# Kernel optimization log

Measured on AMD Instinct MI355X. Metric: run time of the kernel, lower is better.

Reference implementation:

```python
import jax, jax.numpy as jnp
import numpy as np
from jax import lax

DIM = 192
HEADS = 8
B, H, W = 8, 128, 128


def dwconv3x3(x, w):
    # x: [B,C,H,W], w: [C,1,3,3] depthwise (groups=C)
    return lax.conv_general_dilated(
        x, w, window_strides=(1, 1), padding='SAME',
        feature_group_count=x.shape[1],
        dimension_numbers=('NCHW', 'OIHW', 'NCHW'))


def conv1x1(x, w, b=None):
    # w: [Cout, Cin]
    y = jnp.einsum('oc,bchw->bohw', w, x)
    if b is not None:
        y = y + b[None, :, None, None]
    return y


def setup_inputs() -> dict:
    key = jax.random.key(0)
    ks = jax.random.split(key, 9)
    s = 0.02
    return {
        'x': jax.random.normal(ks[0], (B, DIM, H, W), jnp.float32),
        'w_qkv': jax.random.normal(ks[1], (3 * DIM, DIM), jnp.float32) * s,
        'b_qkv': jnp.zeros((3 * DIM,), jnp.float32),
        'w_dw': jax.random.normal(ks[2], (3 * DIM, 1, 3, 3), jnp.float32) * s,
        'b_dw': jnp.zeros((3 * DIM,), jnp.float32),
        'w_proj': jax.random.normal(ks[3], (DIM, DIM), jnp.float32) * s,
        'b_proj': jnp.zeros((DIM,), jnp.float32),
        'w_pos1': jax.random.normal(ks[4], (DIM, 1, 3, 3), jnp.float32) * s,
        'w_pos2': jax.random.normal(ks[5], (DIM, 1, 3, 3), jnp.float32) * s,
        'temperature': jnp.ones((HEADS, 1, 1), jnp.float32),
    }


def reference(x, w_qkv, b_qkv, w_dw, b_dw, w_proj, b_proj, w_pos1, w_pos2, temperature):
    b, c, h, w = x.shape
    heads = HEADS
    ch = c // heads

    qkv = conv1x1(x, w_qkv, b_qkv)
    qkv = dwconv3x3(qkv, w_dw) + b_dw[None, :, None, None]
    q_inp, k_inp, v_inp = jnp.split(qkv, 3, axis=1)

    def to_heads(t):  # [B,C,H,W] -> [B,heads,ch,HW]
        return t.reshape(b, heads, ch, h * w)

    q = to_heads(q_inp)
    k = to_heads(k_inp)
    v = to_heads(v_inp)

    # L2 normalize over hw (torch F.normalize, eps=1e-12)
    q = q / jnp.maximum(jnp.linalg.norm(q, axis=-1, keepdims=True), 1e-12)
    k = k / jnp.maximum(jnp.linalg.norm(k, axis=-1, keepdims=True), 1e-12)

    attn = jnp.einsum('bhce,bhde->bhcd', q, k) * temperature  # [B,heads,ch,ch]
    attn = jax.nn.softmax(attn, axis=-1)
    out = jnp.einsum('bhcd,bhde->bhce', attn, v)  # [B,heads,ch,HW]
    out = out.reshape(b, c, h, w)

    out = conv1x1(out, w_proj, b_proj)

    pos = dwconv3x3(v_inp, w_pos1)
    pos = jax.nn.gelu(pos, approximate=False)
    pos = dwconv3x3(pos, w_pos2)

    return out + pos
```

## Files before the change

### kernel.cpp

```cpp
#include <hip/hip_runtime.h>
#include <stdint.h>
#include <stddef.h>

#define NB 8
#define CC 192
#define C3 576
#define HGT 128
#define WID 128
#define HW 16384
#define NH 8
#define QKROW 49152

typedef short bf16x8 __attribute__((ext_vector_type(8)));
typedef float f32x4 __attribute__((ext_vector_type(4)));

__device__ __forceinline__ unsigned short f2bf(float f) {
  unsigned int u = __float_as_uint(f);
  u += 0x7fffu + ((u >> 16) & 1u);
  return (unsigned short)(u >> 16);
}
__device__ __forceinline__ float bf2f(unsigned short h) {
  return __uint_as_float(((unsigned int)h) << 16);
}
__device__ __forceinline__ float bflo(unsigned int v) {
  return __uint_as_float(v << 16);
}
__device__ __forceinline__ float bfhi(unsigned int v) {
  return __uint_as_float(v & 0xffff0000u);
}
__device__ __forceinline__ unsigned int pk2(float a, float b) {
  return (unsigned int)f2bf(a) | ((unsigned int)f2bf(b) << 16);
}
__device__ __forceinline__ void gl_lds16(const void* g, void* l) {
  __builtin_amdgcn_global_load_lds(
      (const __attribute__((address_space(1))) unsigned int*)(uintptr_t)g,
      (__attribute__((address_space(3))) unsigned int*)(uint32_t)(uintptr_t)l,
      16, 0, 0);
}
__device__ __forceinline__ int xcd_swz(int g, int n) {
  return (g & 7) * (n >> 3) + (g >> 3);
}

__global__ __launch_bounds__(256) void ktrans(const float* __restrict__ x,
                                              unsigned char* __restrict__ xT) {
  __shared__ __align__(16) float lx[192 * 68];
  int wg = xcd_swz(blockIdx.x, gridDim.x);
  int pt = wg & 255, b = wg >> 8;
  int p0 = pt * 64;
  int tid = threadIdx.x;
#pragma unroll
  for (int i = 0; i < 12; ++i) {
    int f = tid + i * 256;
    int ic = f >> 4, q = f & 15;
    float4 v = *(const float4*)(x + ((size_t)(b * CC + ic)) * HW + p0 + q * 4);
    *(float4*)(lx + ic * 68 + q * 4) = v;
  }
  __syncthreads();
#pragma unroll
  for (int i = 0; i < 6; ++i) {
    int f = i * 256 + tid;
    int s = f >> 6, p = f & 63;
    unsigned int wv[4];
#pragma unroll
    for (int j = 0; j < 4; ++j)
      wv[j] = pk2(lx[(s * 8 + 2 * j) * 68 + p], lx[(s * 8 + 2 * j + 1) * 68 + p]);
    uint4 st; st.x = wv[0]; st.y = wv[1]; st.z = wv[2]; st.w = wv[3];
    *(uint4*)(xT + (((size_t)(b * 24 + s)) * HW + p0 + p) * 16) = st;
  }
}

__global__ void kwprep(const float* __restrict__ wq, unsigned char* __restrict__ wb) {
  int f = blockIdx.x * 256 + threadIdx.x;
  if (f >= C3 * 24) return;
  int oc = f / 24, s = f % 24;
  unsigned int wv[4];
#pragma unroll
  for (int j = 0; j < 4; ++j)
    wv[j] = pk2(wq[oc * 192 + s * 8 + 2 * j], wq[oc * 192 + s * 8 + 2 * j + 1]);
  uint4 st; st.x = wv[0]; st.y = wv[1]; st.z = wv[2]; st.w = wv[3];
  *(uint4*)(wb + (size_t)oc * 384 + ((s ^ (oc & 7)) * 16)) = st;
}

__global__ __launch_bounds__(256) void kconv1(const unsigned char* __restrict__ xT,
                                              const unsigned char* __restrict__ wb,
                                              const float* __restrict__ bqkv,
                                              unsigned short* __restrict__ vout,
                                              unsigned char* __restrict__ qkout) {
  __shared__ __align__(16) unsigned char lds[81920];
  const int TRO = 73728;
  int wg = xcd_swz(blockIdx.x, gridDim.x);
  int ot = wg % 9; int rest = wg / 9; int grp = rest & 63; int b = rest >> 6;
  int tid = threadIdx.x;
  const unsigned char* gB = wb + (size_t)ot * 24576;
#pragma unroll
  for (int i = 0; i < 6; ++i)
    gl_lds16(gB + i * 4096 + tid * 16, lds + 49152 + i * 4096 + tid * 16);
  const unsigned char* gA = xT + (size_t)b * 24 * HW * 16;
  int t0 = grp * 4;
  {
    int p0 = t0 * 64;
#pragma unroll
    for (int i = 0; i < 6; ++i) {
      int f = i * 256 + tid;
      gl_lds16(gA + (((size_t)(f >> 6)) * HW + p0 + (f & 63)) * 16, lds + f * 16);
    }
  }
  int lane = tid & 63, w = tid >> 6;
  int l15 = lane & 15, gq = lane >> 4;
  int pw = w * 16;
  int part = ot / 3, cm0 = (ot % 3) * 64;
  bool isq = (ot < 6);
  float bias[4];
#pragma unroll
  for (int nf = 0; nf < 4; ++nf) bias[nf] = bqkv[ot * 64 + nf * 16 + l15];
  size_t vbase[4];
  if (!isq) {
#pragma unroll
    for (int nf = 0; nf < 4; ++nf)
      vbase[nf] = ((size_t)(b * CC + cm0 + nf * 16 + l15)) * HW * 2;
  }
  unsigned char* qkbase = qkout + ((size_t)((part * 8 + b) * 128)) * QKROW;
  int unitw = w * 2 + (gq >> 1);
  int sub8 = (gq & 1) * 8;

  for (int it = 0; it < 4; ++it) {
    int tile = t0 + it;
    asm volatile("s_waitcnt vmcnt(0)" ::: "memory");
    __syncthreads();
    int nb = it & 1;
    if (it < 3) {
      int p1 = (tile + 1) * 64;
#pragma unroll
      for (int i = 0; i < 6; ++i) {
        int f = i * 256 + tid;
        gl_lds16(gA + (((size_t)(f >> 6)) * HW + p1 + (f & 63)) * 16,
                 lds + ((nb ^ 1) * 24576) + f * 16);
      }
    }
    f32x4 acc[4];
#pragma unroll
    for (int nf = 0; nf < 4; ++nf) acc[nf] = (f32x4){0.f, 0.f, 0.f, 0.f};
#pragma unroll
    for (int kk = 0; kk < 6; ++kk) {
      bf16x8 a = *(const bf16x8*)(lds + nb * 24576 + ((((kk * 4 + gq) << 6) + pw + l15) * 16));
      int cb = kk * 64 + gq * 16;
#pragma unroll
      for (int nf = 0; nf < 4; ++nf) {
        int r = nf * 16 + l15;
        bf16x8 bfr = *(const bf16x8*)(lds + 49152 + r * 384 + (cb ^ ((r & 7) << 4)));
        acc[nf] = __builtin_amdgcn_mfma_f32_16x16x32_bf16(a, bfr, acc[nf], 0, 0, 0);
      }
    }
    if (isq) {
#pragma unroll
      for (int nf = 0; nf < 4; ++nf) {
        int c = nf * 16 + l15;
        uint2 st;
        st.x = pk2(acc[nf][0] + bias[nf], acc[nf][1] + bias[nf]);
        st.y = pk2(acc[nf][2] + bias[nf], acc[nf][3] + bias[nf]);
        *(uint2*)(lds + TRO + c * 128 + ((unitw ^ (c & 7)) * 16) + sub8) = st;
      }
      asm volatile("s_waitcnt lgkmcnt(0)" ::: "memory");
      __builtin_amdgcn_s_barrier();
      {
        int y = tile >> 1, xh = (tile & 1) * 8;
        int u = tid >> 5, c0 = tid & 31, c1 = c0 + 32;
        uint4 v0 = *(const uint4*)(lds + TRO + c0 * 128 + ((u ^ (c0 & 7)) * 16));
        uint4 v1 = *(const uint4*)(lds + TRO + c1 * 128 + ((u ^ (c1 & 7)) * 16));
        unsigned char* grow = qkbase + (size_t)y * QKROW + (xh + u) * 3072 + cm0 * 16;
        *(uint4*)(grow + c0 * 16) = v0;
        *(uint4*)(grow + c1 * 16) = v1;
      }
    } else {
      int p = tile * 64 + pw + gq * 4;
#pragma unroll
      for (int nf = 0; nf < 4; ++nf) {
        uint2 st;
        st.x = pk2(acc[nf][0] + bias[nf], acc[nf][1] + bias[nf]);
        st.y = pk2(acc[nf][2] + bias[nf], acc[nf][3] + bias[nf]);
        *(uint2*)((unsigned char*)vout + vbase[nf] + (size_t)p * 2) = st;
      }
    }
  }
}

__global__ __launch_bounds__(256) void kqk(const unsigned char* __restrict__ qk,
                                           const float* __restrict__ wdw,
                                           const float* __restrict__ bdw,
                                           float* __restrict__ G,
                                           float* __restrict__ nq,
                                           float* __restrict__ nk) {
  __shared__ __align__(16) unsigned char lds[81920];
  const int FB = 49152;
  int wg = xcd_swz(blockIdx.x, gridDim.x);
  int band = wg & 63, h = (wg >> 6) & 7, b = wg >> 9;
  int y0 = band * 2;
  int tid = threadIdx.x;
#pragma unroll
  for (int i = 0; i < 12; ++i) {
    int f = i * 256 + tid;
    int p = f / 1536, rem = f % 1536;
    int r = rem / 384, unit = rem % 384;
    int uc = unit / 24, ch = unit % 24;
    int y = y0 - 1 + r;
    if (y >= 0 && y < HGT)
      gl_lds16(qk + ((size_t)((p * 8 + b) * 128 + y)) * QKROW + uc * 3072 + (h * 24 + ch) * 16,
               lds + f * 16);
    else
      *(uint4*)(lds + f * 16) = (uint4){0, 0, 0, 0};
  }
  asm volatile("s_waitcnt vmcnt(0)" ::: "memory");
  __syncthreads();

  int lane = tid & 63, w = tid >> 6;
  if (tid < 192) {
    int p = tid / 96; int r3m = tid % 96;
    int ch = r3m >> 2; int row = (r3m >> 1) & 1; int half = r3m & 1;
    int gc = p * 192 + h * 24 + ch;
    float wv[9];
#pragma unroll
    for (int j = 0; j < 9; ++j) wv[j] = wdw[gc * 9 + j];
    float bias = bdw[gc];
    const unsigned char* sbase = lds + p * 24576 + ch * 16;
    unsigned char* fb = lds + FB + p * 16384 + ch * 16;
    int h8 = half * 8;
    unsigned int W[3][16];
#define LOADU(dy_, m_, u_) { \
    uint4 tt = ((u_) >= 0 && (u_) < 16) \
        ? *(const uint4*)(sbase + (row + (dy_)) * 6144 + (u_) * 384) \
        : (uint4){0, 0, 0, 0}; \
    W[dy_][(m_) * 4 + 0] = tt.x; W[dy_][(m_) * 4 + 1] = tt.y; \
    W[dy_][(m_) * 4 + 2] = tt.z; W[dy_][(m_) * 4 + 3] = tt.w; }
#pragma unroll
    for (int dy = 0; dy < 3; ++dy) {
#pragma unroll
      for (int m = 0; m < 4; ++m) { LOADU(dy, m, h8 - 1 + m); }
    }
    float nsum = 0.f;
#pragma unroll
    for (int c4 = 0; c4 < 4; ++c4) {
      if (c4 > 0) {
#pragma unroll
        for (int dy = 0; dy < 3; ++dy) {
#pragma unroll
          for (int e = 0; e < 8; ++e) W[dy][e] = W[dy][8 + e];
          LOADU(dy, 2, h8 - 1 + c4 * 2 + 2);
          LOADU(dy, 3, h8 - 1 + c4 * 2 + 3);
        }
      }
      float acc[16];
#pragma unroll
      for (int j = 0; j < 16; ++j) acc[j] = bias;
#pragma unroll
      for (int dy = 0; dy < 3; ++dy) {
        float f[18];
#pragma unroll
        for (int t2 = 0; t2 < 18; ++t2) {
          int rel = 7 + t2;
          unsigned int v = W[dy][rel >> 1];
          f[t2] = (rel & 1) ? bfhi(v) : bflo(v);
        }
#pragma unroll
        for (int j = 0; j < 16; ++j)
          acc[j] += f[j] * wv[dy * 3] + f[j + 1] * wv[dy * 3 + 1] + f[j + 2] * wv[dy * 3 + 2];
      }
#pragma unroll
      for (int j = 0; j < 16; ++j) nsum += acc[j] * acc[j];
      unsigned int pk[8];
#pragma unroll
      for (int e = 0; e < 8; ++e) pk[e] = pk2(acc[2 * e], acc[2 * e + 1]);
      int kt = row * 4 + half * 2 + (c4 >> 1);
      int gb = (c4 & 1) * 2;
      uint4 s0; s0.x = pk[0]; s0.y = pk[1]; s0.z = pk[2]; s0.w = pk[3];
      uint4 s1; s1.x = pk[4]; s1.y = pk[5]; s1.z = pk[6]; s1.w = pk[7];
      *(uint4*)(fb + kt * 2048 + gb * 512) = s0;
      *(uint4*)(fb + kt * 2048 + (gb + 1) * 512) = s1;
    }
#undef LOADU
    nsum += __shfl_xor(nsum, 1);
    nsum += __shfl_xor(nsum, 2);
    if ((tid & 3) == 0) {
      float* dst = (p == 0) ? nq : nk;
      atomicAdd(dst + (b * NH + h) * 24 + ch, nsum);
    }
  } else {
    int t2 = tid - 192;
#pragma unroll
    for (int i = 0; i < 8; ++i) {
      int f = i * 64 + t2;
      int ch8 = f & 7, gq4 = (f >> 3) & 3, kt8 = (f >> 5) & 7, pp = f >> 8;
      *(uint4*)(lds + FB + pp * 16384 + kt8 * 2048 + gq4 * 512 + (24 + ch8) * 16) =
          (uint4){0, 0, 0, 0};
    }
  }
  __syncthreads();

  int l15 = lane & 15, gq = lane >> 4;
  f32x4 acc2[2][2];
#pragma unroll
  for (int ct = 0; ct < 2; ++ct)
#pragma unroll
    for (int dt = 0; dt < 2; ++dt) acc2[ct][dt] = (f32x4){0.f, 0.f, 0.f, 0.f};
#pragma unroll
  for (int t2 = 0; t2 < 2; ++t2) {
    int kt = w * 2 + t2;
    bf16x8 aq[2], bk[2];
#pragma unroll
    for (int ct = 0; ct < 2; ++ct) {
      aq[ct] = *(const bf16x8*)(lds + FB + kt * 2048 + gq * 512 + (ct * 16 + l15) * 16);
      bk[ct] = *(const bf16x8*)(lds + FB + 16384 + kt * 2048 + gq * 512 + (ct * 16 + l15) * 16);
    }
#pragma unroll
    for (int ct = 0; ct < 2; ++ct)
#pragma unroll
      for (int dt = 0; dt < 2; ++dt)
        acc2[ct][dt] = __builtin_amdgcn_mfma_f32_16x16x32_bf16(aq[ct], bk[dt], acc2[ct][dt], 0, 0, 0);
  }
  float* gp = (float*)lds;
#pragma unroll
  for (int ct = 0; ct < 2; ++ct)
#pragma unroll
    for (int dt = 0; dt < 2; ++dt)
      *(f32x4*)(gp + (((w * 4 + ct * 2 + dt) * 64) + lane) * 4) = acc2[ct][dt];
  __syncthreads();
  float* Gb = G + (size_t)(b * NH + h) * 576;
#pragma unroll
  for (int ii = 0; ii < 3; ++ii) {
    int f = ii * 256 + tid;
    if (f < 576) {
      int c = f / 24, d = f % 24;
      int t4 = ((c >> 4) << 1) + (d >> 4);
      int lane16 = (d & 15) + (((c & 15) >> 2) << 4);
      int reg = c & 3;
      float s = 0.f;
#pragma unroll
      for (int w4 = 0; w4 < 4; ++w4)
        s += gp[((w4 * 4 + t4) * 64 + lane16) * 4 + reg];
      atomicAdd(Gb + f, s);
    }
  }
}

__global__ __launch_bounds__(256) void kdwv(const unsigned short* __restrict__ src,
                                            const float* __restrict__ wdw,
                                            const float* __restrict__ bdw,
                                            unsigned char* __restrict__ vT) {
  __shared__ __align__(16) unsigned int smem[8 * 721];
  int wg = xcd_swz(blockIdx.x, gridDim.x);
  int cg = wg % 24, rt = (wg / 24) & 15, b = wg / 384;
  int y0 = rt * 8, chg0 = cg * 8;
  int tid = threadIdx.x;
  for (int i = tid; i < 5768; i += 256) smem[i] = 0;
  __syncthreads();
#pragma unroll
  for (int i = 0; i < 5; ++i) {
    int f = i * 256 + tid;
    int ch = f / 160, rem = f % 160;
    int r = rem >> 4, seg = rem & 15;
    int y = y0 - 1 + r;
    if (y >= 0 && y < HGT) {
      uint4 v = *(const uint4*)(src + ((size_t)(b * CC + chg0 + ch)) * HW + y * WID + seg * 8);
      unsigned int* dp = smem + ch * 721 + r * 72 + 4 + seg * 4;
      dp[0] = v.x; dp[1] = v.y; dp[2] = v.z; dp[3] = v.w;
    }
  }
  __syncthreads();
  int ch = tid >> 5, u = tid & 31;
  int row = u >> 2, xs = (u & 3) * 32;
  int gch = 384 + chg0 + ch;
  float wv[9];
#pragma unroll
  for (int j = 0; j < 9; ++j) wv[j] = wdw[gch * 9 + j];
  float bias = bdw[gch];
  float outv[32];
  const unsigned int* tb = smem + ch * 721;
#pragma unroll
  for (int g = 0; g < 4; ++g) {
    int x0 = xs + g * 8;
    float v[3][12];
#pragma unroll
    for (int dy = 0; dy < 3; ++dy) {
      const unsigned int* rp = tb + (row + dy) * 72 + ((x0 + 6) >> 1);
#pragma unroll
      for (int m = 0; m < 6; ++m) {
        unsigned int w2 = rp[m];
        v[dy][2 * m] = bf2f((unsigned short)(w2 & 0xffff));
        v[dy][2 * m + 1] = bf2f((unsigned short)(w2 >> 16));
      }
    }
#pragma unroll
    for (int j = 0; j < 8; ++j) {
      float a = bias;
#pragma unroll
      for (int dy = 0; dy < 3; ++dy)
#pragma unroll
        for (int dx = 0; dx < 3; ++dx)
          a += v[dy][j + dx + 1] * wv[dy * 3 + dx];
      outv[g * 8 + j] = a;
    }
  }
  __syncthreads();
  unsigned short* vt = (unsigned short*)smem;
#pragma unroll
  for (int g = 0; g < 4; ++g)
#pragma unroll
    for (int j = 0; j < 8; j += 2) {
      int x = xs + g * 8 + j;
      ((unsigned int*)smem)[ch * 512 + row * 64 + (x >> 1)] =
          pk2(outv[g * 8 + j], outv[g * 8 + j + 1]);
    }
  __syncthreads();
#pragma unroll
  for (int i = 0; i < 4; ++i) {
    int f = i * 256 + tid;
    int r = f >> 7, col = f & 127;
    unsigned int wvp[4];
#pragma unroll
    for (int e = 0; e < 4; ++e) {
      unsigned short a = vt[(2 * e) * 1024 + r * 128 + col];
      unsigned short bb = vt[(2 * e + 1) * 1024 + r * 128 + col];
      wvp[e] = (unsigned int)a | ((unsigned int)bb << 16);
    }
    uint4 st; st.x = wvp[0]; st.y = wvp[1]; st.z = wvp[2]; st.w = wvp[3];
    *(uint4*)(vT + (((size_t)(b * 24 + cg)) * HW + (size_t)(y0 + r) * WID + col) * 16) = st;
  }
}

__global__ __launch_bounds__(256) void kattn(const float* __restrict__ G,
                                             const float* __restrict__ nq,
                                             const float* __restrict__ nk,
                                             const float* __restrict__ temp,
                                             const float* __restrict__ wproj,
                                             unsigned char* __restrict__ W2) {
  __shared__ float attn[24][24];
  __shared__ float iq[24], ik[24];
  int bh = blockIdx.x;
  int h = bh & 7, b = bh >> 3;
  int tid = threadIdx.x;
  const float* Gb = G + (size_t)bh * 576;
  if (tid < 24) { float n = sqrtf(nq[bh * 24 + tid]); iq[tid] = 1.f / fmaxf(n, 1e-12f); }
  else if (tid < 48) { float n = sqrtf(nk[bh * 24 + tid - 24]); ik[tid - 24] = 1.f / fmaxf(n, 1e-12f); }
  __syncthreads();
  if (tid < 24) {
    float tmp = temp[h];
    float row[24];
    float mx = -1e30f;
#pragma unroll
    for (int d = 0; d < 24; ++d) {
      row[d] = Gb[tid * 24 + d] * iq[tid] * ik[d] * tmp;
      mx = fmaxf(mx, row[d]);
    }
    float sum = 0.f;
#pragma unroll
    for (int d = 0; d < 24; ++d) { float e = expf(row[d] - mx); row[d] = e; sum += e; }
    float inv = 1.f / sum;
#pragma unroll
    for (int d = 0; d < 24; ++d) attn[tid][d] = row[d] * inv;
  }
  __syncthreads();
  for (int i = 0; i < 18; ++i) {
    int f = tid + i * 256;
    if (f >= 4608) break;
    int oc = f / 24, d = f % 24;
    float s = 0.f;
#pragma unroll
    for (int c = 0; c < 24; ++c) s += wproj[oc * 192 + h * 24 + c] * attn[c][d];
    int gg = h * 24 + d;
    *(unsigned short*)(W2 + ((size_t)b * CC + oc) * 384 + ((gg * 2) ^ ((oc & 7) << 4))) = f2bf(s);
  }
}

__global__ __launch_bounds__(256) void kpos(const unsigned char* __restrict__ vT,
                                            const float* __restrict__ w1,
                                            const float* __restrict__ w2,
                                            unsigned short* __restrict__ pos) {
  __shared__ unsigned int vbuf[8 * 865];
  __shared__ unsigned int d1[8 * 721];
  int wg = xcd_swz(blockIdx.x, gridDim.x);
  int cg = wg % 24, rt = (wg / 24) & 15, b = wg / 384;
  int y0 = rt * 8, g0 = cg * 8;
  int tid = threadIdx.x;
  for (int i = tid; i < 6920; i += 256) vbuf[i] = 0;
  __syncthreads();
#pragma unroll
  for (int i = 0; i < 3; ++i) {
    int f = i * 256 + tid;
    int r = f >> 6, colp = f & 63;
    int y = y0 - 2 + r;
    if (y >= 0 && y < HGT) {
      const unsigned char* base = vT + (((size_t)(b * 24 + cg)) * HW + (size_t)y * WID + colp * 2) * 16;
      uint4 va = *(const uint4*)(base);
      uint4 vb2 = *(const uint4*)(base + 16);
      unsigned int la[4] = {va.x, va.y, va.z, va.w};
      unsigned int lb[4] = {vb2.x, vb2.y, vb2.z, vb2.w};
#pragma unroll
      for (int e = 0; e < 8; ++e) {
        unsigned int a16 = (la[e >> 1] >> ((e & 1) * 16)) & 0xffff;
        unsigned int b16 = (lb[e >> 1] >> ((e & 1) * 16)) & 0xffff;
        vbuf[e * 865 + r * 72 + colp + 4] = a16 | (b16 << 16);
      }
    }
  }
  __syncthreads();
  int ch = tid >> 5, u = tid & 31;
  {
    const float* wp = w1 + (g0 + ch) * 9;
    float wl[9];
#pragma unroll
    for (int j = 0; j < 9; ++j) wl[j] = wp[j];
    int x0 = u * 4;
    for (int rr = 0; rr < 10; ++rr) {
      int y = y0 - 1 + rr;
      unsigned int o0 = 0, o1 = 0;
      if (y >= 0 && y < HGT) {
        float v[3][8];
#pragma unroll
        for (int dy = 0; dy < 3; ++dy) {
          const unsigned int* rp = vbuf + ch * 865 + (rr + dy) * 72 + ((x0 + 6) >> 1);
#pragma unroll
          for (int m = 0; m < 4; ++m) {
            unsigned int w2r = rp[m];
            v[dy][2 * m] = bf2f((unsigned short)(w2r & 0xffff));
            v[dy][2 * m + 1] = bf2f((unsigned short)(w2r >> 16));
          }
        }
        float g4[4];
#pragma unroll
        for (int j = 0; j < 4; ++j) {
          float a = 0.f;
#pragma unroll
          for (int dy = 0; dy < 3; ++dy)
#pragma unroll
            for (int dx = 0; dx < 3; ++dx)
              a += v[dy][j + dx + 1] * wl[dy * 3 + dx];
          g4[j] = 0.5f * a * (1.f + erff(a * 0.70710678118f));
        }
        o0 = pk2(g4[0], g4[1]);
        o1 = pk2(g4[2], g4[3]);
      }
      unsigned int* dp = d1 + ch * 721 + rr * 72 + ((x0 + 8) >> 1);
      dp[0] = o0; dp[1] = o1;
    }
  }
  if (tid < 160) {
    int ech = tid / 20, rem = tid % 20;
    int rr = rem >> 1, side = rem & 1;
    int x = side ? 128 : -1;
    int y = y0 - 1 + rr;
    unsigned short val = 0;
    if (y >= 0 && y < HGT) {
      const float* wp = w1 + (g0 + ech) * 9;
      float a = 0.f;
      const unsigned short* vb16 = (const unsigned short*)(vbuf + ech * 865);
#pragma unroll
      for (int dy = 0; dy < 3; ++dy)
#pragma unroll
        for (int dx = 0; dx < 3; ++dx)
          a += bf2f(vb16[(rr + dy) * 144 + (x + dx + 7)]) * wp[dy * 3 + dx];
      val = f2bf(0.5f * a * (1.f + erff(a * 0.70710678118f)));
    }
    ((unsigned short*)(d1 + ech * 721))[rr * 144 + (x + 8)] = val;
  }
  __syncthreads();
  {
    const float* wp = w2 + (g0 + ch) * 9;
    float wl[9];
#pragma unroll
    for (int j = 0; j < 9; ++j) wl[j] = wp[j];
    int row = u >> 2, xs = (u & 3) * 32;
    size_t rb = ((size_t)(b * CC + g0 + ch)) * HW + (size_t)(y0 + row) * WID;
#pragma unroll
    for (int g = 0; g < 4; ++g) {
      int x0 = xs + g * 8;
      float v[3][12];
#pragma unroll
      for (int dy = 0; dy < 3; ++dy) {
        const unsigned int* rp = d1 + ch * 721 + (row + dy) * 72 + ((x0 + 6) >> 1);
#pragma unroll
        for (int m = 0; m < 6; ++m) {
          unsigned int w2r = rp[m];
          v[dy][2 * m] = bf2f((unsigned short)(w2r & 0xffff));
          v[dy][2 * m + 1] = bf2f((unsigned short)(w2r >> 16));
        }
      }
      uint4 st;
      float o[8];
#pragma unroll
      for (int j = 0; j < 8; ++j) {
        float a = 0.f;
#pragma unroll
        for (int dy = 0; dy < 3; ++dy)
#pragma unroll
          for (int dx = 0; dx < 3; ++dx)
            a += v[dy][j + dx + 1] * wl[dy * 3 + dx];
        o[j] = a;
      }
      st.x = pk2(o[0], o[1]); st.y = pk2(o[2], o[3]);
      st.z = pk2(o[4], o[5]); st.w = pk2(o[6], o[7]);
      *(uint4*)(pos + rb + x0) = st;
    }
  }
}

__global__ __launch_bounds__(256) void kproj(const unsigned char* __restrict__ vT,
                                             const unsigned char* __restrict__ W2,
                                             const float* __restrict__ bproj,
                                             const unsigned short* __restrict__ pos,
                                             float* __restrict__ out) {
  __shared__ __align__(16) unsigned char lds[73728];
  int wg = xcd_swz(blockIdx.x, gridDim.x);
  int ot = wg % 3; int rest = wg / 3; int grp = rest & 63; int b = rest >> 6;
  int tid = threadIdx.x;
  const unsigned char* gB = W2 + ((size_t)(b * 192 + ot * 64)) * 384;
#pragma unroll
  for (int i = 0; i < 6; ++i)
    gl_lds16(gB + i * 4096 + tid * 16, lds + 49152 + i * 4096 + tid * 16);
  const unsigned char* gA = vT + (size_t)b * 24 * HW * 16;
  int t0 = grp * 4;
  {
    int p0 = t0 * 64;
#pragma unroll
    for (int i = 0; i < 6; ++i) {
      int f = i * 256 + tid;
      gl_lds16(gA + (((size_t)(f >> 6)) * HW + p0 + (f & 63)) * 16, lds + f * 16);
    }
  }
  int lane = tid & 63, w = tid >> 6;
  int l15 = lane & 15, gq = lane >> 4;
  int pw = w * 16;
  float bias[4];
  size_t obase[4];
#pragma unroll
  for (int nf = 0; nf < 4; ++nf) {
    int oc = ot * 64 + nf * 16 + l15;
    bias[nf] = bproj[oc];
    obase[nf] = ((size_t)(b * 192 + oc)) * HW;
  }
  for (int it = 0; it < 4; ++it) {
    int tile = t0 + it;
    asm volatile("s_waitcnt vmcnt(0)" ::: "memory");
    __syncthreads();
    int nb = it & 1;
    if (it < 3) {
      int p1 = (tile + 1) * 64;
#pragma unroll
      for (int i = 0; i < 6; ++i) {
        int f = i * 256 + tid;
        gl_lds16(gA + (((size_t)(f >> 6)) * HW + p1 + (f & 63)) * 16,
                 lds + ((nb ^ 1) * 24576) + f * 16);
      }
    }
    f32x4 acc[4];
#pragma unroll
    for (int nf = 0; nf < 4; ++nf) acc[nf] = (f32x4){0.f, 0.f, 0.f, 0.f};
#pragma unroll
    for (int kk = 0; kk < 6; ++kk) {
      bf16x8 a = *(const bf16x8*)(lds + nb * 24576 + ((((kk * 4 + gq) << 6) + pw + l15) * 16));
      int cb = kk * 64 + gq * 16;
#pragma unroll
      for (int nf = 0; nf < 4; ++nf) {
        int r = nf * 16 + l15;
        bf16x8 bfr = *(const bf16x8*)(lds + 49152 + r * 384 + (cb ^ ((r & 7) << 4)));
        acc[nf] = __builtin_amdgcn_mfma_f32_16x16x32_bf16(a, bfr, acc[nf], 0, 0, 0);
      }
    }
    int p = tile * 64 + pw + gq * 4;
#pragma unroll
    for (int nf = 0; nf < 4; ++nf) {
      uint2 pv = *(const uint2*)(pos + obase[nf] + p);
      float4 o;
      o.x = acc[nf][0] + bias[nf] + bf2f((unsigned short)(pv.x & 0xffff));
      o.y = acc[nf][1] + bias[nf] + bf2f((unsigned short)(pv.x >> 16));
      o.z = acc[nf][2] + bias[nf] + bf2f((unsigned short)(pv.y & 0xffff));
      o.w = acc[nf][3] + bias[nf] + bf2f((unsigned short)(pv.y >> 16));
      *(float4*)(out + obase[nf] + p) = o;
    }
  }
}

#define OFF_W   ((size_t)0)
#define OFF_G   ((size_t)221184)
#define OFF_NQ  ((size_t)368640)
#define OFF_NK  ((size_t)374784)
#define OFF_W2  ((size_t)380928)
#define OFF_QK  ((size_t)970752)
#define OFF_V   ((size_t)101634048)
#define OFF_XT  ((size_t)151965696)

extern "C" void kernel_launch(void* const* d_in, const int* in_sizes, int n_in,
                              void* d_out, int out_size, void* d_ws, size_t ws_size,
                              hipStream_t stream) {
  const float* x     = (const float*)d_in[0];
  const float* wqkv  = (const float*)d_in[1];
  const float* bqkv  = (const float*)d_in[2];
  const float* wdw   = (const float*)d_in[3];
  const float* bdw   = (const float*)d_in[4];
  const float* wproj = (const float*)d_in[5];
  const float* bproj = (const float*)d_in[6];
  const float* wpos1 = (const float*)d_in[7];
  const float* wpos2 = (const float*)d_in[8];
  const float* temp  = (const float*)d_in[9];
  unsigned char* ws = (unsigned char*)d_ws;

  hipMemsetAsync(ws + OFF_G, 0, 147456 + 6144 + 6144, stream);
  kwprep<<<54, 256, 0, stream>>>(wqkv, ws + OFF_W);
  ktrans<<<2048, 256, 0, stream>>>(x, ws + OFF_XT);
  kconv1<<<4608, 256, 0, stream>>>(ws + OFF_XT, ws + OFF_W, bqkv,
                                   (unsigned short*)(ws + OFF_V), ws + OFF_QK);
  kqk<<<4096, 256, 0, stream>>>(ws + OFF_QK, wdw, bdw, (float*)(ws + OFF_G),
                                (float*)(ws + OFF_NQ), (float*)(ws + OFF_NK));
  kdwv<<<3072, 256, 0, stream>>>((const unsigned short*)(ws + OFF_V), wdw, bdw,
                                 ws + OFF_XT);
  kattn<<<64, 256, 0, stream>>>((const float*)(ws + OFF_G), (const float*)(ws + OFF_NQ),
                                (const float*)(ws + OFF_NK), temp, wproj, ws + OFF_W2);
  kpos<<<3072, 256, 0, stream>>>(ws + OFF_XT, wpos1, wpos2,
                                 (unsigned short*)(ws + OFF_QK));
  kproj<<<1536, 256, 0, stream>>>(ws + OFF_XT, ws + OFF_W2, bproj,
                                  (const unsigned short*)(ws + OFF_QK), (float*)d_out);
}
```

Before: 308.8 us.

## Fuse input transpose into QKV 1x1 conv and loop over output tiles

Removes the separate transpose kernel that wrote a bf16 transposed copy of x to global memory. Each block now loads a 64-pixel fp32 tile of x directly into LDS, converts and transposes it in LDS, and then loops over all 9 output-channel tiles, double-buffering the weight tiles. V outputs are staged through LDS so they can be written with wider coalesced stores. This cuts global traffic for the intermediate xT and the repeated A-tile reloads, at the cost of serial per-block work and fewer blocks.

```diff
diff --git a/kernel.cpp b/kernel.cpp
--- a/kernel.cpp
+++ b/kernel.cpp
@@ -41,34 +41,6 @@
   return (g & 7) * (n >> 3) + (g >> 3);
 }
 
-__global__ __launch_bounds__(256) void ktrans(const float* __restrict__ x,
-                                              unsigned char* __restrict__ xT) {
-  __shared__ __align__(16) float lx[192 * 68];
-  int wg = xcd_swz(blockIdx.x, gridDim.x);
-  int pt = wg & 255, b = wg >> 8;
-  int p0 = pt * 64;
-  int tid = threadIdx.x;
-#pragma unroll
-  for (int i = 0; i < 12; ++i) {
-    int f = tid + i * 256;
-    int ic = f >> 4, q = f & 15;
-    float4 v = *(const float4*)(x + ((size_t)(b * CC + ic)) * HW + p0 + q * 4);
-    *(float4*)(lx + ic * 68 + q * 4) = v;
-  }
-  __syncthreads();
-#pragma unroll
-  for (int i = 0; i < 6; ++i) {
-    int f = i * 256 + tid;
-    int s = f >> 6, p = f & 63;
-    unsigned int wv[4];
-#pragma unroll
-    for (int j = 0; j < 4; ++j)
-      wv[j] = pk2(lx[(s * 8 + 2 * j) * 68 + p], lx[(s * 8 + 2 * j + 1) * 68 + p]);
-    uint4 st; st.x = wv[0]; st.y = wv[1]; st.z = wv[2]; st.w = wv[3];
-    *(uint4*)(xT + (((size_t)(b * 24 + s)) * HW + p0 + p) * 16) = st;
-  }
-}
-
 __global__ void kwprep(const float* __restrict__ wq, unsigned char* __restrict__ wb) {
   int f = blockIdx.x * 256 + threadIdx.x;
   if (f >= C3 * 24) return;
@@ -81,76 +53,88 @@
   *(uint4*)(wb + (size_t)oc * 384 + ((s ^ (oc & 7)) * 16)) = st;
 }
 
-__global__ __launch_bounds__(256) void kconv1(const unsigned char* __restrict__ xT,
-                                              const unsigned char* __restrict__ wb,
-                                              const float* __restrict__ bqkv,
-                                              unsigned short* __restrict__ vout,
-                                              unsigned char* __restrict__ qkout) {
+__global__ __launch_bounds__(256) void kqkv(const float* __restrict__ x,
+                                            const unsigned char* __restrict__ wb,
+                                            const float* __restrict__ bqkv,
+                                            unsigned short* __restrict__ vout,
+                                            unsigned char* __restrict__ qkout) {
   __shared__ __align__(16) unsigned char lds[81920];
+  const int ABF = 49152;
   const int TRO = 73728;
   int wg = xcd_swz(blockIdx.x, gridDim.x);
-  int ot = wg % 9; int rest = wg / 9; int grp = rest & 63; int b = rest >> 6;
+  int t = wg & 255, b = wg >> 8;
+  int p0 = t * 64;
   int tid = threadIdx.x;
-  const unsigned char* gB = wb + (size_t)ot * 24576;
+
+  const unsigned char* gx = (const unsigned char*)(x + (size_t)b * CC * HW + p0);
+#pragma unroll
+  for (int i = 0; i < 12; ++i) {
+    int f = i * 256 + tid;
+    int ch = f >> 4, seg = f & 15;
+    gl_lds16(gx + ((size_t)ch * HW + seg * 4) * 4, lds + f * 16);
+  }
+  asm volatile("s_waitcnt vmcnt(0)" ::: "memory");
+  __syncthreads();
+  {
+    const float* lx = (const float*)lds;
+    int p = tid & 63, sg = tid >> 6;
+#pragma unroll
+    for (int s6 = 0; s6 < 6; ++s6) {
+      int s = sg * 6 + s6;
+      unsigned int wv[4];
+#pragma unroll
+      for (int j = 0; j < 4; ++j)
+        wv[j] = pk2(lx[(s * 8 + 2 * j) * 64 + p], lx[(s * 8 + 2 * j + 1) * 64 + p]);
+      uint4 st; st.x = wv[0]; st.y = wv[1]; st.z = wv[2]; st.w = wv[3];
+      *(uint4*)(lds + ABF + (s * 64 + p) * 16) = st;
+    }
+  }
+  __syncthreads();
+
 #pragma unroll
   for (int i = 0; i < 6; ++i)
-    gl_lds16(gB + i * 4096 + tid * 16, lds + 49152 + i * 4096 + tid * 16);
-  const unsigned char* gA = xT + (size_t)b * 24 * HW * 16;
-  int t0 = grp * 4;
-  {
-    int p0 = t0 * 64;
-#pragma unroll
-    for (int i = 0; i < 6; ++i) {
-      int f = i * 256 + tid;
-      gl_lds16(gA + (((size_t)(f >> 6)) * HW + p0 + (f & 63)) * 16, lds + f * 16);
-    }
-  }
+    gl_lds16(wb + i * 4096 + tid * 16, lds + i * 4096 + tid * 16);
+
   int lane = tid & 63, w = tid >> 6;
   int l15 = lane & 15, gq = lane >> 4;
   int pw = w * 16;
-  int part = ot / 3, cm0 = (ot % 3) * 64;
-  bool isq = (ot < 6);
-  float bias[4];
-#pragma unroll
-  for (int nf = 0; nf < 4; ++nf) bias[nf] = bqkv[ot * 64 + nf * 16 + l15];
-  size_t vbase[4];
-  if (!isq) {
-#pragma unroll
-    for (int nf = 0; nf < 4; ++nf)
-      vbase[nf] = ((size_t)(b * CC + cm0 + nf * 16 + l15)) * HW * 2;
-  }
-  unsigned char* qkbase = qkout + ((size_t)((part * 8 + b) * 128)) * QKROW;
+  int y = t >> 1, xh = (t & 1) * 8;
   int unitw = w * 2 + (gq >> 1);
   int sub8 = (gq & 1) * 8;
-
-  for (int it = 0; it < 4; ++it) {
-    int tile = t0 + it;
-    asm volatile("s_waitcnt vmcnt(0)" ::: "memory");
-    __syncthreads();
-    int nb = it & 1;
-    if (it < 3) {
-      int p1 = (tile + 1) * 64;
-#pragma unroll
-      for (int i = 0; i < 6; ++i) {
-        int f = i * 256 + tid;
-        gl_lds16(gA + (((size_t)(f >> 6)) * HW + p1 + (f & 63)) * 16,
-                 lds + ((nb ^ 1) * 24576) + f * 16);
-      }
+  int s4 = w * 4 + gq;
+  int ru = tid >> 5, rc0 = tid & 31;
+  int vc = tid >> 2, vxq = tid & 3;
+
+  for (int ot = 0; ot < 9; ++ot) {
+    if (ot == 0) { asm volatile("s_waitcnt vmcnt(0)" ::: "memory"); }
+    else         { asm volatile("s_waitcnt vmcnt(2)" ::: "memory"); }
+    __builtin_amdgcn_s_barrier();
+    __builtin_amdgcn_sched_barrier(0);
+    int nb = ot & 1;
+    float bias[4];
+#pragma unroll
+    for (int nf = 0; nf < 4; ++nf) bias[nf] = bqkv[ot * 64 + nf * 16 + l15];
+    if (ot < 8) {
+      const unsigned char* gB = wb + (size_t)(ot + 1) * 24576;
+#pragma unroll
+      for (int i = 0; i < 6; ++i)
+        gl_lds16(gB + i * 4096 + tid * 16, lds + (nb ^ 1) * 24576 + i * 4096 + tid * 16);
     }
     f32x4 acc[4];
 #pragma unroll
     for (int nf = 0; nf < 4; ++nf) acc[nf] = (f32x4){0.f, 0.f, 0.f, 0.f};
 #pragma unroll
     for (int kk = 0; kk < 6; ++kk) {
-      bf16x8 a = *(const bf16x8*)(lds + nb * 24576 + ((((kk * 4 + gq) << 6) + pw + l15) * 16));
+      bf16x8 a = *(const bf16x8*)(lds + ABF + (((kk * 4 + gq) * 64) + pw + l15) * 16);
       int cb = kk * 64 + gq * 16;
 #pragma unroll
       for (int nf = 0; nf < 4; ++nf) {
         int r = nf * 16 + l15;
-        bf16x8 bfr = *(const bf16x8*)(lds + 49152 + r * 384 + (cb ^ ((r & 7) << 4)));
+        bf16x8 bfr = *(const bf16x8*)(lds + nb * 24576 + r * 384 + (cb ^ ((r & 7) << 4)));
         acc[nf] = __builtin_amdgcn_mfma_f32_16x16x32_bf16(a, bfr, acc[nf], 0, 0, 0);
       }
     }
+    bool isq = (ot < 6);
     if (isq) {
 #pragma unroll
       for (int nf = 0; nf < 4; ++nf) {
@@ -160,26 +144,38 @@
         st.y = pk2(acc[nf][2] + bias[nf], acc[nf][3] + bias[nf]);
         *(uint2*)(lds + TRO + c * 128 + ((unitw ^ (c & 7)) * 16) + sub8) = st;
       }
-      asm volatile("s_waitcnt lgkmcnt(0)" ::: "memory");
-      __builtin_amdgcn_s_barrier();
-      {
-        int y = tile >> 1, xh = (tile & 1) * 8;
-        int u = tid >> 5, c0 = tid & 31, c1 = c0 + 32;
-        uint4 v0 = *(const uint4*)(lds + TRO + c0 * 128 + ((u ^ (c0 & 7)) * 16));
-        uint4 v1 = *(const uint4*)(lds + TRO + c1 * 128 + ((u ^ (c1 & 7)) * 16));
-        unsigned char* grow = qkbase + (size_t)y * QKROW + (xh + u) * 3072 + cm0 * 16;
-        *(uint4*)(grow + c0 * 16) = v0;
-        *(uint4*)(grow + c1 * 16) = v1;
-      }
     } else {
-      int p = tile * 64 + pw + gq * 4;
 #pragma unroll
       for (int nf = 0; nf < 4; ++nf) {
+        int c = nf * 16 + l15;
         uint2 st;
         st.x = pk2(acc[nf][0] + bias[nf], acc[nf][1] + bias[nf]);
         st.y = pk2(acc[nf][2] + bias[nf], acc[nf][3] + bias[nf]);
-        *(uint2*)((unsigned char*)vout + vbase[nf] + (size_t)p * 2) = st;
-      }
+        *(uint2*)(lds + TRO + c * 128 + ((s4 ^ (c & 15)) * 8)) = st;
+      }
+    }
+    asm volatile("s_waitcnt lgkmcnt(0)" ::: "memory");
+    __builtin_amdgcn_s_barrier();
+    __builtin_amdgcn_sched_barrier(0);
+    if (isq) {
+      int part = ot / 3, cm0 = (ot % 3) * 64;
+      int c1 = rc0 + 32;
+      uint4 v0 = *(const uint4*)(lds + TRO + rc0 * 128 + ((ru ^ (rc0 & 7)) * 16));
+      uint4 v1 = *(const uint4*)(lds + TRO + c1 * 128 + ((ru ^ (c1 & 7)) * 16));
+      unsigned char* grow = qkout + ((size_t)((part * 8 + b) * 128 + y)) * QKROW +
+                            (xh + ru) * 3072 + cm0 * 16;
+      *(uint4*)(grow + rc0 * 16) = v0;
+      *(uint4*)(grow + c1 * 16) = v1;
+    } else {
+      uint2 q0 = *(const uint2*)(lds + TRO + vc * 128 + (((4 * vxq + 0) ^ (vc & 15)) * 8));
+      uint2 q1 = *(const uint2*)(lds + TRO + vc * 128 + (((4 * vxq + 1) ^ (vc & 15)) * 8));
+      uint2 q2 = *(const uint2*)(lds + TRO + vc * 128 + (((4 * vxq + 2) ^ (vc & 15)) * 8));
+      uint2 q3 = *(const uint2*)(lds + TRO + vc * 128 + (((4 * vxq + 3) ^ (vc & 15)) * 8));
+      unsigned short* vp = vout + ((size_t)(b * CC + (ot - 6) * 64 + vc)) * HW + p0 + vxq * 16;
+      uint4 s0; s0.x = q0.x; s0.y = q0.y; s0.z = q1.x; s0.w = q1.y;
+      uint4 s1; s1.x = q2.x; s1.y = q2.y; s1.z = q3.x; s1.w = q3.y;
+      *(uint4*)vp = s0;
+      *(uint4*)(vp + 8) = s1;
     }
   }
 }
@@ -704,9 +700,8 @@
 
   hipMemsetAsync(ws + OFF_G, 0, 147456 + 6144 + 6144, stream);
   kwprep<<<54, 256, 0, stream>>>(wqkv, ws + OFF_W);
-  ktrans<<<2048, 256, 0, stream>>>(x, ws + OFF_XT);
-  kconv1<<<4608, 256, 0, stream>>>(ws + OFF_XT, ws + OFF_W, bqkv,
-                                   (unsigned short*)(ws + OFF_V), ws + OFF_QK);
+  kqkv<<<2048, 256, 0, stream>>>(x, ws + OFF_W, bqkv,
+                                 (unsigned short*)(ws + OFF_V), ws + OFF_QK);
   kqk<<<4096, 256, 0, stream>>>(ws + OFF_QK, wdw, bdw, (float*)(ws + OFF_G),
                                 (float*)(ws + OFF_NQ), (float*)(ws + OFF_NK));
   kdwv<<<3072, 256, 0, stream>>>((const unsigned short*)(ws + OFF_V), wdw, bdw,
```

Measured after the change: 289.3 us. -6.3%, faster.
